# Performance work log

Hardware: AMD Instinct MI355X
Metric: run time of the kernel (lower is better)

Reference implementation:

```python
import jax, jax.numpy as jnp
import numpy as np

B, N, M, G, F = 8, 1000, 64, 50, 128


def setup_inputs() -> dict:
    key = jax.random.key(0)
    ks = jax.random.split(key, 9)
    s = 0.05
    return {
        "features": jax.random.normal(ks[0], (B, N, F), jnp.float32),
        "rbf_expansion": jax.random.uniform(ks[1], (B, N, M, G), jnp.float32),
        "neighbor_list": jax.random.randint(ks[2], (B, N, M), 0, N, jnp.int64),
        "W_init": jax.random.normal(ks[3], (F, F), jnp.float32) * s,
        "W1": jax.random.normal(ks[4], (G, F), jnp.float32) * s,
        "b1": jnp.zeros((F,), jnp.float32),
        "W2": jax.random.normal(ks[5], (F, F), jnp.float32) * s,
        "b2": jnp.zeros((F,), jnp.float32),
        "nbr_w": jax.random.normal(ks[6], (F,), jnp.float32) * s,
        "Wo1": jax.random.normal(ks[7], (F, F), jnp.float32) * s,
        "bo1": jnp.zeros((F,), jnp.float32),
        "Wo2": jax.random.normal(ks[8], (F, F), jnp.float32) * s,
        "bo2": jnp.zeros((F,), jnp.float32),
    }


def reference(features, rbf_expansion, neighbor_list, W_init, W1, b1, W2, b2,
              nbr_w, Wo1, bo1, Wo2, bo2):
    b, n, m = neighbor_list.shape
    # 1. atom-wise linear, no bias/activation: [B,N,F]
    init = features @ W_init
    # 2. CFConv: filter generator on RBF expansion -> [B,N,M,F]
    filt = jnp.tanh(rbf_expansion @ W1 + b1) @ W2 + b2
    # gather neighbor features: init[b, neighbor_list[b,n,m], :] -> [B,N,M,F]
    idx = neighbor_list.reshape(b, n * m, 1)
    nbr_feat = jnp.take_along_axis(init, idx, axis=1).reshape(b, n, m, -1)
    conv = nbr_feat * filt
    # attention over neighbors via learned vector nbr_w
    attn = jax.nn.softmax(jnp.einsum('bnmf,f->bnm', conv, nbr_w), axis=-1)
    agg = jnp.einsum('bnm,bnmf->bnf', attn, conv)
    # 3-4. output dense: linear+tanh, then linear
    out = jnp.tanh(agg @ Wo1 + bo1) @ Wo2 + bo2
    return out, attn
```

## Files before the change

### kernel.cpp

```cpp
#include <hip/hip_runtime.h>
#include <hip/hip_bf16.h>

typedef __attribute__((ext_vector_type(8))) short short8;
typedef __attribute__((ext_vector_type(4))) float f32x4;
typedef unsigned short u16;
typedef unsigned int u32;

#define NBATCH 8
#define NA 1000
#define MD 64
#define GD 50
#define FD 128
#define TOTAL (NBATCH * NA)

__device__ __forceinline__ u16 f2bf(float f) {
    u32 x = __float_as_uint(f);
    return (u16)((x + 0x7fffu + ((x >> 16) & 1u)) >> 16);
}
__device__ __forceinline__ float bf2f(u16 u) {
    return __uint_as_float(((u32)u) << 16);
}
__device__ __forceinline__ u32 pkbf(float x, float y) {
    __hip_bfloat162 h = __float22bfloat162_rn(float2{x, y});
    return *reinterpret_cast<u32*>(&h);
}
__device__ __forceinline__ float tanh_fast(float x) {
    float e = __expf(2.0f * x);
    return 1.0f - 2.0f * __builtin_amdgcn_rcpf(e + 1.0f);
}
__device__ __forceinline__ f32x4 mfma16(short8 a, short8 b, f32x4 c) {
    return __builtin_amdgcn_mfma_f32_16x16x32_bf16(a, b, c, 0, 0, 0);
}

__global__ void k0_prep(const float* __restrict__ W1, const float* __restrict__ W2,
                        const float* __restrict__ Wi, const float* __restrict__ Wo1,
                        const float* __restrict__ Wo2,
                        u16* __restrict__ W1P, u16* __restrict__ W2P,
                        u16* __restrict__ WiP, u16* __restrict__ Wo1P,
                        u16* __restrict__ Wo2P) {
    const int g0 = blockIdx.x * 256 + threadIdx.x;
    const int gstep = gridDim.x * 256;
    for (int p = g0; p < 16 * 512; p += gstep) {
        int seg = p >> 9, l = (p >> 3) & 63, j = p & 7;
        int ks = seg >> 3, nt = seg & 7;
        int k = ks * 32 + ((l >> 4) << 3) + j;
        int n = nt * 16 + (l & 15);
        W1P[p] = (k < GD) ? f2bf(W1[k * FD + n]) : (u16)0;
    }
    for (int p = g0; p < 32 * 512; p += gstep) {
        int seg = p >> 9, l = (p >> 3) & 63, j = p & 7;
        int half = seg >> 4, ks = (seg >> 3) & 1, nt = seg & 7;
        int kstor = half * 64 + ks * 32 + ((l >> 4) << 3) + j;
        int n = nt * 16 + (l & 15);
        WiP[p]  = f2bf(Wi[kstor * FD + n]);
        Wo1P[p] = f2bf(Wo1[kstor * FD + n]);
        int kperm = (kstor >> 3) | ((kstor & 7) << 4);
        W2P[p]  = f2bf(W2[kperm * FD + n]);
        Wo2P[p] = f2bf(Wo2[kperm * FD + n]);
    }
}

__global__ __launch_bounds__(64) void k1_init(const float* __restrict__ feat,
                                              const u16* __restrict__ WiP,
                                              u16* __restrict__ initB) {
    const int lane = threadIdx.x;
    const int quad = lane >> 4, col = lane & 15;
    const int row0 = blockIdx.x * 16;

    f32x4 acc[8];
    const f32x4 zf = {0.f, 0.f, 0.f, 0.f};
#pragma unroll
    for (int nt = 0; nt < 8; ++nt) acc[nt] = zf;

#pragma unroll
    for (int half = 0; half < 2; ++half)
#pragma unroll
        for (int ks = 0; ks < 2; ++ks) {
            const int ka = half * 64 + ks * 32 + quad * 8;
            const float* src = &feat[(size_t)(row0 + col) * FD + ka];
            float4 v0 = *(const float4*)src;
            float4 v1 = *(const float4*)(src + 4);
            short8 a;
            u32* ap = (u32*)&a;
            ap[0] = pkbf(v0.x, v0.y);
            ap[1] = pkbf(v0.z, v0.w);
            ap[2] = pkbf(v1.x, v1.y);
            ap[3] = pkbf(v1.z, v1.w);
#pragma unroll
            for (int nt = 0; nt < 8; ++nt) {
                short8 bfr = *(const short8*)&WiP[(((half * 2 + ks) * 8 + nt) << 9) + (lane << 3)];
                acc[nt] = mfma16(a, bfr, acc[nt]);
            }
        }
#pragma unroll
    for (int r = 0; r < 4; ++r) {
        short8 g;
        u32* gp = (u32*)&g;
        gp[0] = pkbf(acc[0][r], acc[1][r]);
        gp[1] = pkbf(acc[2][r], acc[3][r]);
        gp[2] = pkbf(acc[4][r], acc[5][r]);
        gp[3] = pkbf(acc[6][r], acc[7][r]);
        *(short8*)&initB[(size_t)(row0 + quad * 4 + r) * FD + col * 8] = g;
    }
}

__global__ __launch_bounds__(256, 4) void k2_main(
    const float* __restrict__ rbf, const int* __restrict__ nl,
    const u16* __restrict__ initB,
    const u16* __restrict__ W1P, const u16* __restrict__ W2P,
    const float* __restrict__ b1, const float* __restrict__ b2,
    const float* __restrict__ nbrw,
    float* __restrict__ aggOut, float* __restrict__ attnO) {
    __shared__ alignas(16) char smem[34816];
    const int tid = threadIdx.x, wid = tid >> 6, lane = tid & 63;
    const int quad = lane >> 4, col = lane & 15, rw = wid * 32;
    const int blk = blockIdx.x;
    const int b = blk / 500;
    const int n0 = (blk - b * 500) * 2;
    const int atom0 = b * NA + n0;

    u16* wv = (u16*)smem + wid * 4352;
    float* logitS = (float*)smem;
    float* aggS   = (float*)(smem + 1024);

    int rowoff[2][4];
#pragma unroll
    for (int mt = 0; mt < 2; ++mt)
#pragma unroll
        for (int r = 0; r < 4; ++r)
            rowoff[mt][r] = (b * NA + nl[atom0 * MD + rw + mt * 16 + quad * 4 + r]) * FD;

    {
        const float* rsrc = rbf + (size_t)(atom0 * MD + rw) * GD;
        for (int i = lane; i < 800; i += 64) {
            int e = 2 * i;
            int r = e / 50, g = e - r * 50;
            float2 v = *(const float2*)&rsrc[e];
            *(u32*)&wv[r * 68 + g] = pkbf(v.x, v.y);
        }
        for (int i = lane; i < 448; i += 64) {
            int r = i / 14;
            wv[r * 68 + 50 + (i - r * 14)] = 0;
        }
    }

    f32x4 acc[2][8];
#pragma unroll
    for (int nt = 0; nt < 8; ++nt) {
        float bb = b1[nt * 16 + col];
        f32x4 c = {bb, bb, bb, bb};
        acc[0][nt] = c;
        acc[1][nt] = c;
    }
#pragma unroll
    for (int ks = 0; ks < 2; ++ks) {
        const int ka = ks * 32 + quad * 8;
        short8 a0 = *(const short8*)&wv[col * 68 + ka];
        short8 a1 = *(const short8*)&wv[(16 + col) * 68 + ka];
#pragma unroll
        for (int nt = 0; nt < 8; ++nt) {
            short8 bfr = *(const short8*)&W1P[((ks * 8 + nt) << 9) + (lane << 3)];
            acc[0][nt] = mfma16(a0, bfr, acc[0][nt]);
            acc[1][nt] = mfma16(a1, bfr, acc[1][nt]);
        }
    }

#pragma unroll
    for (int mt = 0; mt < 2; ++mt)
#pragma unroll
        for (int r = 0; r < 4; ++r) {
            short8 h;
            u32* hp = (u32*)&h;
            hp[0] = pkbf(tanh_fast(acc[mt][0][r]), tanh_fast(acc[mt][1][r]));
            hp[1] = pkbf(tanh_fast(acc[mt][2][r]), tanh_fast(acc[mt][3][r]));
            hp[2] = pkbf(tanh_fast(acc[mt][4][r]), tanh_fast(acc[mt][5][r]));
            hp[3] = pkbf(tanh_fast(acc[mt][6][r]), tanh_fast(acc[mt][7][r]));
            *(short8*)&wv[(mt * 16 + quad * 4 + r) * 136 + col * 8] = h;
        }

    f32x4 acc2[2][8];
#pragma unroll
    for (int nt = 0; nt < 8; ++nt) {
        float bb = b2[nt * 16 + col];
        f32x4 c = {bb, bb, bb, bb};
        acc2[0][nt] = c;
        acc2[1][nt] = c;
    }
#pragma unroll
    for (int half = 0; half < 2; ++half)
#pragma unroll
        for (int ks = 0; ks < 2; ++ks) {
            const int ka = half * 64 + ks * 32 + quad * 8;
            short8 a0 = *(const short8*)&wv[col * 136 + ka];
            short8 a1 = *(const short8*)&wv[(16 + col) * 136 + ka];
#pragma unroll
            for (int nt = 0; nt < 8; ++nt) {
                short8 bfr = *(const short8*)&W2P[(((half * 2 + ks) * 8 + nt) << 9) + (lane << 3)];
                acc2[0][nt] = mfma16(a0, bfr, acc2[0][nt]);
                acc2[1][nt] = mfma16(a1, bfr, acc2[1][nt]);
            }
        }

    float wv8[8];
#pragma unroll
    for (int nt = 0; nt < 8; ++nt) wv8[nt] = nbrw[nt * 16 + col];
    float part[2][4] = {{0.f, 0.f, 0.f, 0.f}, {0.f, 0.f, 0.f, 0.f}};
#pragma unroll
    for (int mt = 0; mt < 2; ++mt)
#pragma unroll
        for (int r = 0; r < 4; ++r) {
            short8 g = *(const short8*)&initB[rowoff[mt][r] + col * 8];
#pragma unroll
            for (int nt = 0; nt < 8; ++nt) {
                float nb = bf2f((u16)g[nt]);
                float cv = nb * acc2[mt][nt][r];
                acc2[mt][nt][r] = cv;
                part[mt][r] += cv * wv8[nt];
            }
        }
#pragma unroll
    for (int d = 1; d < 16; d <<= 1)
#pragma unroll
        for (int mt = 0; mt < 2; ++mt)
#pragma unroll
            for (int r = 0; r < 4; ++r)
                part[mt][r] += __shfl_xor(part[mt][r], d, 64);

    __syncthreads();
    if (col == 0) {
#pragma unroll
        for (int mt = 0; mt < 2; ++mt)
#pragma unroll
            for (int r = 0; r < 4; ++r)
                logitS[rw + mt * 16 + quad * 4 + r] = part[mt][r];
    }
    __syncthreads();

    float attw[2][4];
    {
        const int base = rw & 64;
        float x = logitS[base + lane];
        float m = x;
#pragma unroll
        for (int d = 1; d < 64; d <<= 1) m = fmaxf(m, __shfl_xor(m, d, 64));
        float e = __expf(x - m);
        float s = e;
#pragma unroll
        for (int d = 1; d < 64; d <<= 1) s += __shfl_xor(s, d, 64);
        float a = e / s;
        if ((wid & 1) == 0)
            attnO[(size_t)(atom0 + (wid >> 1)) * MD + lane] = a;
#pragma unroll
        for (int mt = 0; mt < 2; ++mt)
#pragma unroll
            for (int r = 0; r < 4; ++r)
                attw[mt][r] = __shfl(a, (rw & 32) + mt * 16 + quad * 4 + r, 64);
    }

    float aggp[8] = {0.f, 0.f, 0.f, 0.f, 0.f, 0.f, 0.f, 0.f};
#pragma unroll
    for (int mt = 0; mt < 2; ++mt)
#pragma unroll
        for (int r = 0; r < 4; ++r) {
            float a = attw[mt][r];
#pragma unroll
            for (int nt = 0; nt < 8; ++nt) aggp[nt] += a * acc2[mt][nt][r];
        }
#pragma unroll
    for (int d = 16; d < 64; d <<= 1)
#pragma unroll
        for (int nt = 0; nt < 8; ++nt) aggp[nt] += __shfl_xor(aggp[nt], d, 64);
    if (quad == 0) {
#pragma unroll
        for (int nt = 0; nt < 8; ++nt) aggS[wid * 128 + nt * 16 + col] = aggp[nt];
    }
    __syncthreads();
    {
        int a = tid >> 7;
        int c = tid & 127;
        float v = aggS[(2 * a) * 128 + c] + aggS[(2 * a + 1) * 128 + c];
        aggOut[(size_t)(atom0 + a) * FD + c] = v;
    }
}

__global__ __launch_bounds__(64) void k3_out(
    float* __restrict__ outp, const u16* __restrict__ Wo1P,
    const u16* __restrict__ Wo2P, const float* __restrict__ bo1,
    const float* __restrict__ bo2) {
    __shared__ alignas(16) u16 sT[16 * 136];
    const int lane = threadIdx.x;
    const int quad = lane >> 4, col = lane & 15;
    const int row0 = blockIdx.x * 16;

    f32x4 acc[8];
#pragma unroll
    for (int nt = 0; nt < 8; ++nt) {
        float bb = bo1[nt * 16 + col];
        f32x4 c = {bb, bb, bb, bb};
        acc[nt] = c;
    }
#pragma unroll
    for (int half = 0; half < 2; ++half)
#pragma unroll
        for (int ks = 0; ks < 2; ++ks) {
            const int ka = half * 64 + ks * 32 + quad * 8;
            const float* src = &outp[(size_t)(row0 + col) * FD + ka];
            float4 v0 = *(const float4*)src;
            float4 v1 = *(const float4*)(src + 4);
            short8 a;
            u32* ap = (u32*)&a;
            ap[0] = pkbf(v0.x, v0.y);
            ap[1] = pkbf(v0.z, v0.w);
            ap[2] = pkbf(v1.x, v1.y);
            ap[3] = pkbf(v1.z, v1.w);
#pragma unroll
            for (int nt = 0; nt < 8; ++nt) {
                short8 bfr = *(const short8*)&Wo1P[(((half * 2 + ks) * 8 + nt) << 9) + (lane << 3)];
                acc[nt] = mfma16(a, bfr, acc[nt]);
            }
        }

#pragma unroll
    for (int r = 0; r < 4; ++r) {
        short8 h;
        u32* hp = (u32*)&h;
        hp[0] = pkbf(tanh_fast(acc[0][r]), tanh_fast(acc[1][r]));
        hp[1] = pkbf(tanh_fast(acc[2][r]), tanh_fast(acc[3][r]));
        hp[2] = pkbf(tanh_fast(acc[4][r]), tanh_fast(acc[5][r]));
        hp[3] = pkbf(tanh_fast(acc[6][r]), tanh_fast(acc[7][r]));
        *(short8*)&sT[(quad * 4 + r) * 136 + col * 8] = h;
    }
    __syncthreads();

    f32x4 acc2[8];
#pragma unroll
    for (int nt = 0; nt < 8; ++nt) {
        float bb = bo2[nt * 16 + col];
        f32x4 c = {bb, bb, bb, bb};
        acc2[nt] = c;
    }
#pragma unroll
    for (int half = 0; half < 2; ++half)
#pragma unroll
        for (int ks = 0; ks < 2; ++ks) {
            const int ka = half * 64 + ks * 32 + quad * 8;
            short8 a0 = *(const short8*)&sT[col * 136 + ka];
#pragma unroll
            for (int nt = 0; nt < 8; ++nt) {
                short8 bfr = *(const short8*)&Wo2P[(((half * 2 + ks) * 8 + nt) << 9) + (lane << 3)];
                acc2[nt] = mfma16(a0, bfr, acc2[nt]);
            }
        }
#pragma unroll
    for (int nt = 0; nt < 8; ++nt)
#pragma unroll
        for (int r = 0; r < 4; ++r)
            outp[(size_t)(row0 + quad * 4 + r) * FD + nt * 16 + col] = acc2[nt][r];
}

extern "C" void kernel_launch(void* const* d_in, const int* in_sizes, int n_in,
                              void* d_out, int out_size, void* d_ws,
                              size_t ws_size, hipStream_t stream) {
    const float* feat = (const float*)d_in[0];
    const float* rbf  = (const float*)d_in[1];
    const int*   nl   = (const int*)d_in[2];
    const float* Wi   = (const float*)d_in[3];
    const float* W1   = (const float*)d_in[4];
    const float* b1   = (const float*)d_in[5];
    const float* W2   = (const float*)d_in[6];
    const float* b2   = (const float*)d_in[7];
    const float* nbrw = (const float*)d_in[8];
    const float* Wo1  = (const float*)d_in[9];
    const float* bo1  = (const float*)d_in[10];
    const float* Wo2  = (const float*)d_in[11];
    const float* bo2  = (const float*)d_in[12];

    float* outp  = (float*)d_out;
    float* attnp = outp + (size_t)TOTAL * FD;

    char* ws = (char*)d_ws;
    u16* initB = (u16*)ws;
    u16* W1P   = (u16*)(ws + 2048000);
    u16* W2P   = (u16*)(ws + 2064384);
    u16* WiP   = (u16*)(ws + 2097152);
    u16* Wo1P  = (u16*)(ws + 2129920);
    u16* Wo2P  = (u16*)(ws + 2162688);

    hipLaunchKernelGGL(k0_prep, dim3(40), dim3(256), 0, stream,
                       W1, W2, Wi, Wo1, Wo2, W1P, W2P, WiP, Wo1P, Wo2P);
    hipLaunchKernelGGL(k1_init, dim3(500), dim3(64), 0, stream, feat, WiP, initB);
    hipLaunchKernelGGL(k2_main, dim3(4000), dim3(256), 0, stream,
                       rbf, nl, initB, W1P, W2P, b1, b2, nbrw, outp, attnp);
    hipLaunchKernelGGL(k3_out, dim3(500), dim3(64), 0, stream,
                       outp, Wo1P, Wo2P, bo1, bo2);
}
```

Measured before the change: 259.7 us.

## Process one atom per block with 16 neighbors per wave for occupancy

Restructures k2_main so each 256-thread block handles a single atom and each wave handles 16 neighbor rows instead of 32. Per-wave accumulators halve, shared memory halves, and launch bounds rise to 6 blocks per CU, with twice as many blocks launched. The goal is more resident waves to hide the latency of the RBF loads and neighbor gathers. In exchange, each B-fragment load of W1P/W2P is reused by only one MFMA instead of two, and the per-block overhead of bias and weight loads doubles.

```diff
diff --git a/kernel.cpp b/kernel.cpp
--- a/kernel.cpp
+++ b/kernel.cpp
@@ -104,87 +104,77 @@
     }
 }
 
-__global__ __launch_bounds__(256, 4) void k2_main(
+__global__ __launch_bounds__(256, 6) void k2_main(
     const float* __restrict__ rbf, const int* __restrict__ nl,
     const u16* __restrict__ initB,
     const u16* __restrict__ W1P, const u16* __restrict__ W2P,
     const float* __restrict__ b1, const float* __restrict__ b2,
     const float* __restrict__ nbrw,
     float* __restrict__ aggOut, float* __restrict__ attnO) {
-    __shared__ alignas(16) char smem[34816];
+    __shared__ alignas(16) char smem[17408];
     const int tid = threadIdx.x, wid = tid >> 6, lane = tid & 63;
-    const int quad = lane >> 4, col = lane & 15, rw = wid * 32;
-    const int blk = blockIdx.x;
-    const int b = blk / 500;
-    const int n0 = (blk - b * 500) * 2;
-    const int atom0 = b * NA + n0;
-
-    u16* wv = (u16*)smem + wid * 4352;
+    const int quad = lane >> 4, col = lane & 15;
+    const int atom = blockIdx.x;
+    const int b = atom / NA;
+
+    u16* wv = (u16*)smem + wid * 2176;
     float* logitS = (float*)smem;
-    float* aggS   = (float*)(smem + 1024);
-
-    int rowoff[2][4];
-#pragma unroll
-    for (int mt = 0; mt < 2; ++mt)
-#pragma unroll
-        for (int r = 0; r < 4; ++r)
-            rowoff[mt][r] = (b * NA + nl[atom0 * MD + rw + mt * 16 + quad * 4 + r]) * FD;
+    float* aggS   = (float*)(smem + 256);
+
+    int rowoff[4];
+#pragma unroll
+    for (int r = 0; r < 4; ++r)
+        rowoff[r] = (b * NA + nl[atom * MD + wid * 16 + quad * 4 + r]) * FD;
 
     {
-        const float* rsrc = rbf + (size_t)(atom0 * MD + rw) * GD;
-        for (int i = lane; i < 800; i += 64) {
+        const float* rsrc = rbf + (size_t)(atom * MD + wid * 16) * GD;
+        for (int i = lane; i < 400; i += 64) {
             int e = 2 * i;
             int r = e / 50, g = e - r * 50;
             float2 v = *(const float2*)&rsrc[e];
             *(u32*)&wv[r * 68 + g] = pkbf(v.x, v.y);
         }
-        for (int i = lane; i < 448; i += 64) {
+        for (int i = lane; i < 224; i += 64) {
             int r = i / 14;
             wv[r * 68 + 50 + (i - r * 14)] = 0;
         }
     }
 
-    f32x4 acc[2][8];
+    f32x4 acc[8];
 #pragma unroll
     for (int nt = 0; nt < 8; ++nt) {
         float bb = b1[nt * 16 + col];
         f32x4 c = {bb, bb, bb, bb};
-        acc[0][nt] = c;
-        acc[1][nt] = c;
+        acc[nt] = c;
     }
 #pragma unroll
     for (int ks = 0; ks < 2; ++ks) {
         const int ka = ks * 32 + quad * 8;
         short8 a0 = *(const short8*)&wv[col * 68 + ka];
-        short8 a1 = *(const short8*)&wv[(16 + col) * 68 + ka];
 #pragma unroll
         for (int nt = 0; nt < 8; ++nt) {
             short8 bfr = *(const short8*)&W1P[((ks * 8 + nt) << 9) + (lane << 3)];
-            acc[0][nt] = mfma16(a0, bfr, acc[0][nt]);
-            acc[1][nt] = mfma16(a1, bfr, acc[1][nt]);
-        }
-    }
-
-#pragma unroll
-    for (int mt = 0; mt < 2; ++mt)
-#pragma unroll
-        for (int r = 0; r < 4; ++r) {
-            short8 h;
-            u32* hp = (u32*)&h;
-            hp[0] = pkbf(tanh_fast(acc[mt][0][r]), tanh_fast(acc[mt][1][r]));
-            hp[1] = pkbf(tanh_fast(acc[mt][2][r]), tanh_fast(acc[mt][3][r]));
-            hp[2] = pkbf(tanh_fast(acc[mt][4][r]), tanh_fast(acc[mt][5][r]));
-            hp[3] = pkbf(tanh_fast(acc[mt][6][r]), tanh_fast(acc[mt][7][r]));
-            *(short8*)&wv[(mt * 16 + quad * 4 + r) * 136 + col * 8] = h;
-        }
-
-    f32x4 acc2[2][8];
+            acc[nt] = mfma16(a0, bfr, acc[nt]);
+        }
+    }
+
+#pragma unroll
+    for (int r = 0; r < 4; ++r) {
+        short8 h;
+        u32* hp = (u32*)&h;
+        hp[0] = pkbf(tanh_fast(acc[0][r]), tanh_fast(acc[1][r]));
+        hp[1] = pkbf(tanh_fast(acc[2][r]), tanh_fast(acc[3][r]));
+        hp[2] = pkbf(tanh_fast(acc[4][r]), tanh_fast(acc[5][r]));
+        hp[3] = pkbf(tanh_fast(acc[6][r]), tanh_fast(acc[7][r]));
+        *(short8*)&wv[(quad * 4 + r) * 136 + col * 8] = h;
+    }
+
+    f32x4 acc2[8];
 #pragma unroll
     for (int nt = 0; nt < 8; ++nt) {
         float bb = b2[nt * 16 + col];
         f32x4 c = {bb, bb, bb, bb};
-        acc2[0][nt] = c;
-        acc2[1][nt] = c;
+        acc2[nt] = c;
     }
 #pragma unroll
     for (int half = 0; half < 2; ++half)
@@ -192,54 +182,45 @@
         for (int ks = 0; ks < 2; ++ks) {
             const int ka = half * 64 + ks * 32 + quad * 8;
             short8 a0 = *(const short8*)&wv[col * 136 + ka];
-            short8 a1 = *(const short8*)&wv[(16 + col) * 136 + ka];
 #pragma unroll
             for (int nt = 0; nt < 8; ++nt) {
                 short8 bfr = *(const short8*)&W2P[(((half * 2 + ks) * 8 + nt) << 9) + (lane << 3)];
-                acc2[0][nt] = mfma16(a0, bfr, acc2[0][nt]);
-                acc2[1][nt] = mfma16(a1, bfr, acc2[1][nt]);
+                acc2[nt] = mfma16(a0, bfr, acc2[nt]);
             }
         }
 
     float wv8[8];
 #pragma unroll
     for (int nt = 0; nt < 8; ++nt) wv8[nt] = nbrw[nt * 16 + col];
-    float part[2][4] = {{0.f, 0.f, 0.f, 0.f}, {0.f, 0.f, 0.f, 0.f}};
-#pragma unroll
-    for (int mt = 0; mt < 2; ++mt)
-#pragma unroll
-        for (int r = 0; r < 4; ++r) {
-            short8 g = *(const short8*)&initB[rowoff[mt][r] + col * 8];
-#pragma unroll
-            for (int nt = 0; nt < 8; ++nt) {
-                float nb = bf2f((u16)g[nt]);
-                float cv = nb * acc2[mt][nt][r];
-                acc2[mt][nt][r] = cv;
-                part[mt][r] += cv * wv8[nt];
-            }
-        }
+    float part[4] = {0.f, 0.f, 0.f, 0.f};
+#pragma unroll
+    for (int r = 0; r < 4; ++r) {
+        short8 g = *(const short8*)&initB[rowoff[r] + col * 8];
+#pragma unroll
+        for (int nt = 0; nt < 8; ++nt) {
+            float nb = bf2f((u16)g[nt]);
+            float cv = nb * acc2[nt][r];
+            acc2[nt][r] = cv;
+            part[r] += cv * wv8[nt];
+        }
+    }
 #pragma unroll
     for (int d = 1; d < 16; d <<= 1)
 #pragma unroll
-        for (int mt = 0; mt < 2; ++mt)
-#pragma unroll
-            for (int r = 0; r < 4; ++r)
-                part[mt][r] += __shfl_xor(part[mt][r], d, 64);
+        for (int r = 0; r < 4; ++r)
+            part[r] += __shfl_xor(part[r], d, 64);
 
     __syncthreads();
     if (col == 0) {
 #pragma unroll
-        for (int mt = 0; mt < 2; ++mt)
-#pragma unroll
-            for (int r = 0; r < 4; ++r)
-                logitS[rw + mt * 16 + quad * 4 + r] = part[mt][r];
+        for (int r = 0; r < 4; ++r)
+            logitS[wid * 16 + quad * 4 + r] = part[r];
     }
     __syncthreads();
 
-    float attw[2][4];
+    float attw[4];
     {
-        const int base = rw & 64;
-        float x = logitS[base + lane];
+        float x = logitS[lane];
         float m = x;
 #pragma unroll
         for (int d = 1; d < 64; d <<= 1) m = fmaxf(m, __shfl_xor(m, d, 64));
@@ -248,24 +229,19 @@
 #pragma unroll
         for (int d = 1; d < 64; d <<= 1) s += __shfl_xor(s, d, 64);
         float a = e / s;
-        if ((wid & 1) == 0)
-            attnO[(size_t)(atom0 + (wid >> 1)) * MD + lane] = a;
-#pragma unroll
-        for (int mt = 0; mt < 2; ++mt)
-#pragma unroll
-            for (int r = 0; r < 4; ++r)
-                attw[mt][r] = __shfl(a, (rw & 32) + mt * 16 + quad * 4 + r, 64);
+        if (wid == 0) attnO[(size_t)atom * MD + lane] = a;
+#pragma unroll
+        for (int r = 0; r < 4; ++r)
+            attw[r] = __shfl(a, wid * 16 + quad * 4 + r, 64);
     }
 
     float aggp[8] = {0.f, 0.f, 0.f, 0.f, 0.f, 0.f, 0.f, 0.f};
 #pragma unroll
-    for (int mt = 0; mt < 2; ++mt)
-#pragma unroll
-        for (int r = 0; r < 4; ++r) {
-            float a = attw[mt][r];
-#pragma unroll
-            for (int nt = 0; nt < 8; ++nt) aggp[nt] += a * acc2[mt][nt][r];
-        }
+    for (int r = 0; r < 4; ++r) {
+        float a = attw[r];
+#pragma unroll
+        for (int nt = 0; nt < 8; ++nt) aggp[nt] += a * acc2[nt][r];
+    }
 #pragma unroll
     for (int d = 16; d < 64; d <<= 1)
 #pragma unroll
@@ -275,11 +251,9 @@
         for (int nt = 0; nt < 8; ++nt) aggS[wid * 128 + nt * 16 + col] = aggp[nt];
     }
     __syncthreads();
-    {
-        int a = tid >> 7;
-        int c = tid & 127;
-        float v = aggS[(2 * a) * 128 + c] + aggS[(2 * a + 1) * 128 + c];
-        aggOut[(size_t)(atom0 + a) * FD + c] = v;
+    if (tid < 128) {
+        float v = aggS[tid] + aggS[128 + tid] + aggS[256 + tid] + aggS[384 + tid];
+        aggOut[(size_t)atom * FD + tid] = v;
     }
 }
 
@@ -389,7 +363,7 @@
     hipLaunchKernelGGL(k0_prep, dim3(40), dim3(256), 0, stream,
                        W1, W2, Wi, Wo1, Wo2, W1P, W2P, WiP, Wo1P, Wo2P);
     hipLaunchKernelGGL(k1_init, dim3(500), dim3(64), 0, stream, feat, WiP, initB);
-    hipLaunchKernelGGL(k2_main, dim3(4000), dim3(256), 0, stream,
+    hipLaunchKernelGGL(k2_main, dim3(8000), dim3(256), 0, stream,
                        rbf, nl, initB, W1P, W2P, b1, b2, nbrw, outp, attnp);
     hipLaunchKernelGGL(k3_out, dim3(500), dim3(64), 0, stream,
                        outp, Wo1P, Wo2P, bo1, bo2);
```

New measurement: 251.3 us. 3.2% less time.
